# Kernel optimization log

Hardware: AMD Instinct MI355X
Metric: run time of the kernel (lower is better)

## Reference

```python
import math
import jax, jax.numpy as jnp
import numpy as np

HEAD_DIM = 2
ROPE_PERIOD = 19.0
OMEGA = 2.0 * math.pi / ROPE_PERIOD
PEAK_EPS = 0.3
TARGET_LOGIT_GAP = math.log(10.0)
ATTN_AMPLITUDE = TARGET_LOGIT_GAP / (math.cos(OMEGA * PEAK_EPS) - math.cos(OMEGA * (1.0 - PEAK_EPS)))
QK_NORM_SCALE = math.sqrt(ATTN_AMPLITUDE / math.sqrt(2.0))
SCALE = HEAD_DIM ** (-0.5) * QK_NORM_SCALE ** 2
INTERMEDIATE_SIZE = 2
EMBED_CONST = 1000.0
B, L = 4, 4096


def _rms(x, eps=1e-6):
    return x * jax.lax.rsqrt(jnp.mean(x * x, axis=-1, keepdims=True) + eps)


def _rope(x):
    # x: (B, 1, L, 2)
    seq_len = x.shape[2]
    theta = jnp.arange(seq_len, dtype=x.dtype) * jnp.asarray(OMEGA, x.dtype)
    cos_t = jnp.cos(theta)[None, None, :, None]
    sin_t = jnp.sin(theta)[None, None, :, None]
    x0, x1 = x[..., 0:1], x[..., 1:2]
    return jnp.concatenate([x0 * cos_t - x1 * sin_t, x0 * sin_t + x1 * cos_t], axis=-1)


def setup_inputs() -> dict:
    key = jax.random.key(0)
    k1, k2, k3, k4, k5 = jax.random.split(key, 5)
    x = jax.random.normal(k1, (B, L, 2), dtype=jnp.float32)
    # causal additive mask (1, 1, L, L)
    causal = jnp.tril(jnp.ones((L, L), dtype=bool))
    mask = jnp.where(causal, 0.0, -1e9).astype(jnp.float32)[None, None]
    q_weight = jax.random.normal(k2, (1,), dtype=jnp.float32) * 0.1
    v_weight = jax.random.normal(k3, (1,), dtype=jnp.float32) * 0.1
    gate_weight = jax.random.normal(k4, (2,), dtype=jnp.float32) * 0.1
    carry_weight = jax.random.normal(k5, (1,), dtype=jnp.float32) * 0.1
    return {"x": x, "mask": mask, "q_weight": q_weight, "v_weight": v_weight,
            "gate_weight": gate_weight, "carry_weight": carry_weight}


def reference(x, mask, q_weight, v_weight, gate_weight, carry_weight):
    # ---- attention branch ----
    xn = _rms(x)                                    # (B, L, 2)
    phi = q_weight[0]
    q = jnp.stack([xn[..., 0] * jnp.cos(phi), xn[..., 0] * -jnp.sin(phi)], axis=-1)
    k = jnp.stack([xn[..., 0], jnp.zeros_like(xn[..., 0])], axis=-1)
    v = jnp.stack([xn[..., 1] * v_weight[0], jnp.zeros_like(xn[..., 0])], axis=-1)
    q, k, v = q[:, None], k[:, None], v[:, None]    # (B, 1, L, 2)
    q = _rope(_rms(q))
    k = _rope(_rms(k))
    attn = jnp.einsum('bhqd,bhkd->bhqk', q, k) * jnp.asarray(SCALE, x.dtype)
    attn = jax.nn.softmax(attn + mask, axis=-1)
    out = jnp.einsum('bhqk,bhkd->bhqd', attn, v)    # (B, 1, L, 2)
    o0 = out[:, 0, :, 0]                            # (B, L)
    attn_out = jnp.stack([jnp.zeros_like(o0), o0], axis=-1)  # OProj channel swap
    h = x + attn_out
    # ---- gated MLP branch ----
    hn = _rms(h)
    a, c = gate_weight[0], gate_weight[1]
    g0 = hn[..., 0] * a + hn[..., 1] * c
    g1 = hn[..., 0] * (a - c / EMBED_CONST) + hn[..., 1] * c
    base = hn[..., 0]
    mix0 = jax.nn.silu(g0) * base
    mix1 = jax.nn.silu(g1) * base
    y1 = carry_weight[0] * (mix1 - mix0)
    mlp_out = jnp.stack([jnp.zeros_like(y1), y1], axis=-1)
    return h + mlp_out
```

## Files before the change

### kernel.cpp

```cpp
#include <hip/hip_runtime.h>
#include <hip/hip_fp16.h>
#include <math.h>

#define SEQ_L 4096
#define THREADS 512

__device__ __forceinline__ float wave_sum_dpp(float x) {
    int t;
    t = __builtin_amdgcn_update_dpp(0, __float_as_int(x), 0x111, 0xf, 0xf, true); x += __int_as_float(t);
    t = __builtin_amdgcn_update_dpp(0, __float_as_int(x), 0x112, 0xf, 0xf, true); x += __int_as_float(t);
    t = __builtin_amdgcn_update_dpp(0, __float_as_int(x), 0x114, 0xf, 0xf, true); x += __int_as_float(t);
    t = __builtin_amdgcn_update_dpp(0, __float_as_int(x), 0x118, 0xf, 0xf, true); x += __int_as_float(t);
    t = __builtin_amdgcn_update_dpp(0, __float_as_int(x), 0x142, 0xa, 0xf, true); x += __int_as_float(t);
    t = __builtin_amdgcn_update_dpp(0, __float_as_int(x), 0x143, 0xc, 0xf, true); x += __int_as_float(t);
    return x;
}

__device__ __forceinline__ void do_group(
    int g, int lane, const float2* __restrict__ x2, const __half2* aw,
    float2* __restrict__ outp, float scaleL2, float cphi, float sphi,
    float cd, float sd, float ck1, float sk1, float ck2, float sk2,
    float ck3, float sk3, float ga, float gc, float cw)
{
    const float INV19 = 1.0f / 19.0f;
    const float LOG2E = 1.4426950408889634f;

    int m  = g / 19;
    int c  = g - 19 * m;
    int b0 = 76 * m + c;
    int i0r = b0, i1r = b0 + 19, i2r = b0 + 38, i3r = b0 + 57;

    float t2a0, t2a1, t2a2, t2a3, M2a0, M2a1, M2a2, M2a3;
#define ROWINIT(tk, Mk, ik) { \
    int ic_ = (ik) < SEQ_L ? (ik) : (SEQ_L - 1); \
    float2 xv_ = x2[ic_]; \
    float inv_ = __builtin_amdgcn_rsqf(fmaf(xv_.x, xv_.x*0.5f, fmaf(xv_.y, xv_.y*0.5f, 1e-6f))); \
    float xn0_ = xv_.x * inv_; \
    float ai_  = xn0_ * __builtin_amdgcn_rsqf(fmaf(xn0_, xn0_*0.5f, 1e-6f)); \
    tk = scaleL2 * ai_;  Mk = fabsf(tk) * 1.4142135623730951f; }
    ROWINIT(t2a0, M2a0, i0r)
    ROWINIT(t2a1, M2a1, i1r)
    ROWINIT(t2a2, M2a2, i2r)
    ROWINIT(t2a3, M2a3, i3r)
#undef ROWINIT

    unsigned r = (unsigned)(b0 - (lane << 2) + 266) % 19u;
    float rev = (float)r * INV19;
    float crv = __builtin_amdgcn_cosf(rev);
    float srv = __builtin_amdgcn_sinf(rev);
    float C = fmaf(srv, sphi, crv * cphi);
    float S = fmaf(crv, -sphi, srv * cphi);

    float sa0=0.f, sa1=0.f, sa2=0.f, sa3=0.f;
    float oa0=0.f, oa1=0.f, oa2=0.f, oa3=0.f;
    int jb = lane << 2;
    const int ncom = (b0 + 1) >> 8;
    const int i3c  = i3r < SEQ_L ? i3r : (SEQ_L - 1);
    const int T    = (i3c >> 8) + 1;

#define EL(u, pw) { \
    float e0_ = __builtin_amdgcn_exp2f(fmaf(t2a0, (u), -M2a0)); \
    float e1_ = __builtin_amdgcn_exp2f(fmaf(t2a1, (u), -M2a1)); \
    float e2_ = __builtin_amdgcn_exp2f(fmaf(t2a2, (u), -M2a2)); \
    float e3_ = __builtin_amdgcn_exp2f(fmaf(t2a3, (u), -M2a3)); \
    sa0 += e0_; oa0 = fmaf(e0_, (pw), oa0); \
    sa1 += e1_; oa1 = fmaf(e1_, (pw), oa1); \
    sa2 += e2_; oa2 = fmaf(e2_, (pw), oa2); \
    sa3 += e3_; oa3 = fmaf(e3_, (pw), oa3); }
#define ELM(u, pw, jj) { \
    float e0_ = __builtin_amdgcn_exp2f(fmaf(t2a0, (u), -M2a0)); \
    float e1_ = __builtin_amdgcn_exp2f(fmaf(t2a1, (u), -M2a1)); \
    float e2_ = __builtin_amdgcn_exp2f(fmaf(t2a2, (u), -M2a2)); \
    float e3_ = __builtin_amdgcn_exp2f(fmaf(t2a3, (u), -M2a3)); \
    e0_ = ((jj) <= i0r) ? e0_ : 0.f; \
    e1_ = ((jj) <= i1r) ? e1_ : 0.f; \
    e2_ = ((jj) <= i2r) ? e2_ : 0.f; \
    e3_ = ((jj) <= i3r) ? e3_ : 0.f; \
    sa0 += e0_; oa0 = fmaf(e0_, (pw), oa0); \
    sa1 += e1_; oa1 = fmaf(e1_, (pw), oa1); \
    sa2 += e2_; oa2 = fmaf(e2_, (pw), oa2); \
    sa3 += e3_; oa3 = fmaf(e3_, (pw), oa3); }

    int t = 0;
    for (; t < ncom; ++t) {
        float4 raw = *(const float4*)&aw[jb];
        const __half2* hp = (const __half2*)&raw;
        float2 p0 = __half22float2(hp[0]);
        float2 p1 = __half22float2(hp[1]);
        float2 p2 = __half22float2(hp[2]);
        float2 p3 = __half22float2(hp[3]);
        float C1 = fmaf(S, sk1, C * ck1);
        float C2 = fmaf(S, sk2, C * ck2);
        float C3 = fmaf(S, sk3, C * ck3);
        float u0 = p0.x * C,  u1 = p1.x * C1, u2 = p2.x * C2, u3 = p3.x * C3;
        EL(u0, p0.y) EL(u1, p1.y) EL(u2, p2.y) EL(u3, p3.y)
        float Cn = fmaf(S, sd, C * cd);
        float Sn = fmaf(S, cd, -(C * sd));
        C = Cn; S = Sn;
        jb += 256;
    }
    for (; t < T; ++t) {
        float4 raw = *(const float4*)&aw[jb];
        const __half2* hp = (const __half2*)&raw;
        float2 p0 = __half22float2(hp[0]);
        float2 p1 = __half22float2(hp[1]);
        float2 p2 = __half22float2(hp[2]);
        float2 p3 = __half22float2(hp[3]);
        float C1 = fmaf(S, sk1, C * ck1);
        float C2 = fmaf(S, sk2, C * ck2);
        float C3 = fmaf(S, sk3, C * ck3);
        float u0 = p0.x * C,  u1 = p1.x * C1, u2 = p2.x * C2, u3 = p3.x * C3;
        ELM(u0, p0.y, jb)     ELM(u1, p1.y, jb + 1)
        ELM(u2, p2.y, jb + 2) ELM(u3, p3.y, jb + 3)
        float Cn = fmaf(S, sd, C * cd);
        float Sn = fmaf(S, cd, -(C * sd));
        C = Cn; S = Sn;
        jb += 256;
    }
#undef EL
#undef ELM

    float S0 = wave_sum_dpp(sa0), O0 = wave_sum_dpp(oa0);
    float S1 = wave_sum_dpp(sa1), O1 = wave_sum_dpp(oa1);
    float S2 = wave_sum_dpp(sa2), O2 = wave_sum_dpp(oa2);
    float S3 = wave_sum_dpp(sa3), O3 = wave_sum_dpp(oa3);

    if (lane == 63) {
#define EPI(Sk, Ok, ik) if ((ik) < SEQ_L) { \
    float2 xv_ = x2[ik]; \
    float o0_ = (Ok) * __builtin_amdgcn_rcpf(Sk); \
    float h0_ = xv_.x, h1_ = xv_.y + o0_; \
    float inv_ = __builtin_amdgcn_rsqf(fmaf(h0_, h0_*0.5f, fmaf(h1_, h1_*0.5f, 1e-6f))); \
    float hn0_ = h0_ * inv_, hn1_ = h1_ * inv_; \
    float g0_ = hn0_ * ga + hn1_ * gc; \
    float g1_ = hn0_ * (ga - gc * 1e-3f) + hn1_ * gc; \
    float sg0_ = __builtin_amdgcn_rcpf(1.f + __builtin_amdgcn_exp2f(-g0_ * LOG2E)); \
    float sg1_ = __builtin_amdgcn_rcpf(1.f + __builtin_amdgcn_exp2f(-g1_ * LOG2E)); \
    float y1_ = cw * (g1_ * sg1_ - g0_ * sg0_) * hn0_; \
    outp[ik] = make_float2(h0_, h1_ + y1_); }
        EPI(S0, O0, i0r)
        EPI(S1, O1, i1r)
        EPI(S2, O2, i2r)
        EPI(S3, O3, i3r)
#undef EPI
    }
}

__global__ __launch_bounds__(THREADS, 4) void attn_rows_kernel(
    const float* __restrict__ x,
    const float* __restrict__ q_weight,
    const float* __restrict__ v_weight,
    const float* __restrict__ gate_weight,
    const float* __restrict__ carry_weight,
    float* __restrict__ out,
    float scaleL2,
    float cd, float sd,
    float ck1, float sk1, float ck2, float sk2, float ck3, float sk3)
{
    __shared__ __half2 aw[SEQ_L];

    const int tid  = threadIdx.x;
    const int lane = tid & 63;
    const int wave = tid >> 6;
    const int bat  = blockIdx.x >> 7;
    const int bb   = blockIdx.x & 127;

    const float phi = q_weight[0];
    const float vw  = v_weight[0];
    const float2* x2 = (const float2*)x + (size_t)bat * SEQ_L;
    float2* outp = (float2*)out + (size_t)bat * SEQ_L;

    const float INV2PI = 0.15915494309189535f;
    const float rphi = phi * INV2PI;
    const float cphi = __builtin_amdgcn_cosf(rphi);
    const float sphi = __builtin_amdgcn_sinf(rphi);

    for (int j = tid; j < SEQ_L; j += THREADS) {
        float2 xv = x2[j];
        float inv = __builtin_amdgcn_rsqf(
                        fmaf(xv.x, xv.x * 0.5f, fmaf(xv.y, xv.y * 0.5f, 1e-6f)));
        float xn0 = xv.x * inv;
        float xn1 = xv.y * inv;
        float a = xn0 * __builtin_amdgcn_rsqf(fmaf(xn0, xn0 * 0.5f, 1e-6f));
        aw[j] = __floats2half2_rn(a, xn1 * vw);
    }
    __syncthreads();

    const float ga = gate_weight[0];
    const float gc = gate_weight[1];
    const float cw = carry_weight[0];

    const int q = bb + (wave << 7);
    const int g = (q < 513) ? q : (1538 - q);

    do_group(g, lane, x2, aw, outp, scaleL2, cphi, sphi,
             cd, sd, ck1, sk1, ck2, sk2, ck3, sk3, ga, gc, cw);
    if (q == 511)
        do_group(514, lane, x2, aw, outp, scaleL2, cphi, sphi,
                 cd, sd, ck1, sk1, ck2, sk2, ck3, sk3, ga, gc, cw);
    else if (q == 512)
        do_group(513, lane, x2, aw, outp, scaleL2, cphi, sphi,
                 cd, sd, ck1, sk1, ck2, sk2, ck3, sk3, ga, gc, cw);
}

extern "C" void kernel_launch(void* const* d_in, const int* in_sizes, int n_in,
                              void* d_out, int out_size, void* d_ws, size_t ws_size,
                              hipStream_t stream)
{
    const float* x  = (const float*)d_in[0];
    const float* qw = (const float*)d_in[2];
    const float* vw = (const float*)d_in[3];
    const float* gw = (const float*)d_in[4];
    const float* cw = (const float*)d_in[5];
    float* out = (float*)d_out;

    const double omega = 2.0 * M_PI / 19.0;
    const double amp   = log(10.0) / (cos(omega * 0.3) - cos(omega * 0.7));
    const double qkns2 = amp / sqrt(2.0);
    const double scale = pow(2.0, -0.5) * qkns2;
    const double L2E   = 1.4426950408889634074;
    const double delta = 256.0 * omega;

    attn_rows_kernel<<<dim3(4 * 128), dim3(THREADS), 0, stream>>>(
        x, qw, vw, gw, cw, out,
        (float)(scale * L2E),
        (float)cos(delta),       (float)sin(delta),
        (float)cos(omega),       (float)sin(omega),
        (float)cos(2.0 * omega), (float)sin(2.0 * omega),
        (float)cos(3.0 * omega), (float)sin(3.0 * omega));
}
```

Baseline: 18.41 us.

## Store keys and values as fp32 in LDS, pair rows per wave, prefetch tiles

Changes the per-key LDS table from packed half2 to two padded fp32 arrays, removing half-to-float conversions and fp16 rounding. Each wave now handles two complementary row groups (b0 and 4046-b0) so causal work is balanced, and blocks shrink to 256 threads with 129 blocks per batch. The loop software-prefetches the next float4 tile, and row init reads the precomputed normalized values from LDS. In exchange, LDS use doubles and the input staging is done in fewer, wider loads.

```diff
diff --git a/kernel.cpp b/kernel.cpp
--- a/kernel.cpp
+++ b/kernel.cpp
@@ -1,9 +1,8 @@
 #include <hip/hip_runtime.h>
-#include <hip/hip_fp16.h>
 #include <math.h>
 
 #define SEQ_L 4096
-#define THREADS 512
+#define LDS_PAD 260
 
 __device__ __forceinline__ float wave_sum_dpp(float x) {
     int t;
@@ -17,35 +16,28 @@
 }
 
 __device__ __forceinline__ void do_group(
-    int g, int lane, const float2* __restrict__ x2, const __half2* aw,
-    float2* __restrict__ outp, float scaleL2, float cphi, float sphi,
+    int b0, int lane, const float2* __restrict__ x2,
+    const float* As, const float* Ws, float2* __restrict__ outp,
+    float scaleL2, float cphi, float sphi,
     float cd, float sd, float ck1, float sk1, float ck2, float sk2,
     float ck3, float sk3, float ga, float gc, float cw)
 {
-    const float INV19 = 1.0f / 19.0f;
     const float LOG2E = 1.4426950408889634f;
-
-    int m  = g / 19;
-    int c  = g - 19 * m;
-    int b0 = 76 * m + c;
-    int i0r = b0, i1r = b0 + 19, i2r = b0 + 38, i3r = b0 + 57;
-
-    float t2a0, t2a1, t2a2, t2a3, M2a0, M2a1, M2a2, M2a3;
-#define ROWINIT(tk, Mk, ik) { \
-    int ic_ = (ik) < SEQ_L ? (ik) : (SEQ_L - 1); \
-    float2 xv_ = x2[ic_]; \
-    float inv_ = __builtin_amdgcn_rsqf(fmaf(xv_.x, xv_.x*0.5f, fmaf(xv_.y, xv_.y*0.5f, 1e-6f))); \
-    float xn0_ = xv_.x * inv_; \
-    float ai_  = xn0_ * __builtin_amdgcn_rsqf(fmaf(xn0_, xn0_*0.5f, 1e-6f)); \
-    tk = scaleL2 * ai_;  Mk = fabsf(tk) * 1.4142135623730951f; }
-    ROWINIT(t2a0, M2a0, i0r)
-    ROWINIT(t2a1, M2a1, i1r)
-    ROWINIT(t2a2, M2a2, i2r)
-    ROWINIT(t2a3, M2a3, i3r)
-#undef ROWINIT
+    const float SQRT2 = 1.4142135623730951f;
+    const int i0 = b0, i1 = b0 + 19, i2 = b0 + 38, i3 = b0 + 57;
+    const int c1 = i1 < SEQ_L ? i1 : SEQ_L - 1;
+    const int c2 = i2 < SEQ_L ? i2 : SEQ_L - 1;
+    const int c3 = i3 < SEQ_L ? i3 : SEQ_L - 1;
+
+    const float t20 = scaleL2 * As[i0], t21 = scaleL2 * As[c1];
+    const float t22 = scaleL2 * As[c2], t23 = scaleL2 * As[c3];
+    const float M20 = fabsf(t20) * SQRT2, M21 = fabsf(t21) * SQRT2;
+    const float M22 = fabsf(t22) * SQRT2, M23 = fabsf(t23) * SQRT2;
+
+    const float2 xv0 = x2[i0], xv1 = x2[c1], xv2 = x2[c2], xv3 = x2[c3];
 
     unsigned r = (unsigned)(b0 - (lane << 2) + 266) % 19u;
-    float rev = (float)r * INV19;
+    float rev = (float)r * (1.0f / 19.0f);
     float crv = __builtin_amdgcn_cosf(rev);
     float srv = __builtin_amdgcn_sinf(rev);
     float C = fmaf(srv, sphi, crv * cphi);
@@ -55,70 +47,66 @@
     float oa0=0.f, oa1=0.f, oa2=0.f, oa3=0.f;
     int jb = lane << 2;
     const int ncom = (b0 + 1) >> 8;
-    const int i3c  = i3r < SEQ_L ? i3r : (SEQ_L - 1);
-    const int T    = (i3c >> 8) + 1;
-
-#define EL(u, pw) { \
-    float e0_ = __builtin_amdgcn_exp2f(fmaf(t2a0, (u), -M2a0)); \
-    float e1_ = __builtin_amdgcn_exp2f(fmaf(t2a1, (u), -M2a1)); \
-    float e2_ = __builtin_amdgcn_exp2f(fmaf(t2a2, (u), -M2a2)); \
-    float e3_ = __builtin_amdgcn_exp2f(fmaf(t2a3, (u), -M2a3)); \
+    const int T    = (c3 >> 8) + 1;
+
+#define EL4(u, pw) { \
+    float e0_ = __builtin_amdgcn_exp2f(fmaf(t20, (u), -M20)); \
+    float e1_ = __builtin_amdgcn_exp2f(fmaf(t21, (u), -M21)); \
+    float e2_ = __builtin_amdgcn_exp2f(fmaf(t22, (u), -M22)); \
+    float e3_ = __builtin_amdgcn_exp2f(fmaf(t23, (u), -M23)); \
     sa0 += e0_; oa0 = fmaf(e0_, (pw), oa0); \
     sa1 += e1_; oa1 = fmaf(e1_, (pw), oa1); \
     sa2 += e2_; oa2 = fmaf(e2_, (pw), oa2); \
     sa3 += e3_; oa3 = fmaf(e3_, (pw), oa3); }
-#define ELM(u, pw, jj) { \
-    float e0_ = __builtin_amdgcn_exp2f(fmaf(t2a0, (u), -M2a0)); \
-    float e1_ = __builtin_amdgcn_exp2f(fmaf(t2a1, (u), -M2a1)); \
-    float e2_ = __builtin_amdgcn_exp2f(fmaf(t2a2, (u), -M2a2)); \
-    float e3_ = __builtin_amdgcn_exp2f(fmaf(t2a3, (u), -M2a3)); \
-    e0_ = ((jj) <= i0r) ? e0_ : 0.f; \
-    e1_ = ((jj) <= i1r) ? e1_ : 0.f; \
-    e2_ = ((jj) <= i2r) ? e2_ : 0.f; \
-    e3_ = ((jj) <= i3r) ? e3_ : 0.f; \
+#define ELM4(u, pw, jj) { \
+    float e0_ = __builtin_amdgcn_exp2f(fmaf(t20, (u), -M20)); \
+    float e1_ = __builtin_amdgcn_exp2f(fmaf(t21, (u), -M21)); \
+    float e2_ = __builtin_amdgcn_exp2f(fmaf(t22, (u), -M22)); \
+    float e3_ = __builtin_amdgcn_exp2f(fmaf(t23, (u), -M23)); \
+    e0_ = ((jj) <= i0) ? e0_ : 0.f; \
+    e1_ = ((jj) <= i1) ? e1_ : 0.f; \
+    e2_ = ((jj) <= i2) ? e2_ : 0.f; \
+    e3_ = ((jj) <= i3) ? e3_ : 0.f; \
     sa0 += e0_; oa0 = fmaf(e0_, (pw), oa0); \
     sa1 += e1_; oa1 = fmaf(e1_, (pw), oa1); \
     sa2 += e2_; oa2 = fmaf(e2_, (pw), oa2); \
     sa3 += e3_; oa3 = fmaf(e3_, (pw), oa3); }
-
+#define ROT() { \
+    float Cn_ = fmaf(S, sd, C * cd); \
+    float Sn_ = fmaf(S, cd, -(C * sd)); \
+    C = Cn_; S = Sn_; }
+
+    float4 av = *(const float4*)&As[jb];
+    float4 wv = *(const float4*)&Ws[jb];
     int t = 0;
     for (; t < ncom; ++t) {
-        float4 raw = *(const float4*)&aw[jb];
-        const __half2* hp = (const __half2*)&raw;
-        float2 p0 = __half22float2(hp[0]);
-        float2 p1 = __half22float2(hp[1]);
-        float2 p2 = __half22float2(hp[2]);
-        float2 p3 = __half22float2(hp[3]);
+        float4 avn = *(const float4*)&As[jb + 256];
+        float4 wvn = *(const float4*)&Ws[jb + 256];
         float C1 = fmaf(S, sk1, C * ck1);
         float C2 = fmaf(S, sk2, C * ck2);
         float C3 = fmaf(S, sk3, C * ck3);
-        float u0 = p0.x * C,  u1 = p1.x * C1, u2 = p2.x * C2, u3 = p3.x * C3;
-        EL(u0, p0.y) EL(u1, p1.y) EL(u2, p2.y) EL(u3, p3.y)
-        float Cn = fmaf(S, sd, C * cd);
-        float Sn = fmaf(S, cd, -(C * sd));
-        C = Cn; S = Sn;
-        jb += 256;
+        float u0 = av.x * C,  u1 = av.y * C1;
+        float u2 = av.z * C2, u3 = av.w * C3;
+        EL4(u0, wv.x) EL4(u1, wv.y) EL4(u2, wv.z) EL4(u3, wv.w)
+        ROT();
+        av = avn; wv = wvn; jb += 256;
     }
     for (; t < T; ++t) {
-        float4 raw = *(const float4*)&aw[jb];
-        const __half2* hp = (const __half2*)&raw;
-        float2 p0 = __half22float2(hp[0]);
-        float2 p1 = __half22float2(hp[1]);
-        float2 p2 = __half22float2(hp[2]);
-        float2 p3 = __half22float2(hp[3]);
+        float4 avn = *(const float4*)&As[jb + 256];
+        float4 wvn = *(const float4*)&Ws[jb + 256];
         float C1 = fmaf(S, sk1, C * ck1);
         float C2 = fmaf(S, sk2, C * ck2);
         float C3 = fmaf(S, sk3, C * ck3);
-        float u0 = p0.x * C,  u1 = p1.x * C1, u2 = p2.x * C2, u3 = p3.x * C3;
-        ELM(u0, p0.y, jb)     ELM(u1, p1.y, jb + 1)
-        ELM(u2, p2.y, jb + 2) ELM(u3, p3.y, jb + 3)
-        float Cn = fmaf(S, sd, C * cd);
-        float Sn = fmaf(S, cd, -(C * sd));
-        C = Cn; S = Sn;
-        jb += 256;
-    }
-#undef EL
-#undef ELM
+        float u0 = av.x * C,  u1 = av.y * C1;
+        float u2 = av.z * C2, u3 = av.w * C3;
+        ELM4(u0, wv.x, jb)     ELM4(u1, wv.y, jb + 1)
+        ELM4(u2, wv.z, jb + 2) ELM4(u3, wv.w, jb + 3)
+        ROT();
+        av = avn; wv = wvn; jb += 256;
+    }
+#undef EL4
+#undef ELM4
+#undef ROT
 
     float S0 = wave_sum_dpp(sa0), O0 = wave_sum_dpp(oa0);
     float S1 = wave_sum_dpp(sa1), O1 = wave_sum_dpp(oa1);
@@ -126,10 +114,9 @@
     float S3 = wave_sum_dpp(sa3), O3 = wave_sum_dpp(oa3);
 
     if (lane == 63) {
-#define EPI(Sk, Ok, ik) if ((ik) < SEQ_L) { \
-    float2 xv_ = x2[ik]; \
+#define EPI(Sk, Ok, ik, xvk) if ((ik) < SEQ_L) { \
     float o0_ = (Ok) * __builtin_amdgcn_rcpf(Sk); \
-    float h0_ = xv_.x, h1_ = xv_.y + o0_; \
+    float h0_ = (xvk).x, h1_ = (xvk).y + o0_; \
     float inv_ = __builtin_amdgcn_rsqf(fmaf(h0_, h0_*0.5f, fmaf(h1_, h1_*0.5f, 1e-6f))); \
     float hn0_ = h0_ * inv_, hn1_ = h1_ * inv_; \
     float g0_ = hn0_ * ga + hn1_ * gc; \
@@ -138,15 +125,15 @@
     float sg1_ = __builtin_amdgcn_rcpf(1.f + __builtin_amdgcn_exp2f(-g1_ * LOG2E)); \
     float y1_ = cw * (g1_ * sg1_ - g0_ * sg0_) * hn0_; \
     outp[ik] = make_float2(h0_, h1_ + y1_); }
-        EPI(S0, O0, i0r)
-        EPI(S1, O1, i1r)
-        EPI(S2, O2, i2r)
-        EPI(S3, O3, i3r)
+        EPI(S0, O0, i0, xv0)
+        EPI(S1, O1, i1, xv1)
+        EPI(S2, O2, i2, xv2)
+        EPI(S3, O3, i3, xv3)
 #undef EPI
     }
 }
 
-__global__ __launch_bounds__(THREADS, 4) void attn_rows_kernel(
+__global__ __launch_bounds__(256, 4) void attn_rows_kernel(
     const float* __restrict__ x,
     const float* __restrict__ q_weight,
     const float* __restrict__ v_weight,
@@ -157,13 +144,14 @@
     float cd, float sd,
     float ck1, float sk1, float ck2, float sk2, float ck3, float sk3)
 {
-    __shared__ __half2 aw[SEQ_L];
+    __shared__ float As[SEQ_L + LDS_PAD];
+    __shared__ float Ws[SEQ_L + LDS_PAD];
 
     const int tid  = threadIdx.x;
     const int lane = tid & 63;
     const int wave = tid >> 6;
-    const int bat  = blockIdx.x >> 7;
-    const int bb   = blockIdx.x & 127;
+    const int bat  = blockIdx.x / 129;
+    const int bb   = blockIdx.x % 129;
 
     const float phi = q_weight[0];
     const float vw  = v_weight[0];
@@ -175,32 +163,39 @@
     const float cphi = __builtin_amdgcn_cosf(rphi);
     const float sphi = __builtin_amdgcn_sinf(rphi);
 
-    for (int j = tid; j < SEQ_L; j += THREADS) {
-        float2 xv = x2[j];
-        float inv = __builtin_amdgcn_rsqf(
-                        fmaf(xv.x, xv.x * 0.5f, fmaf(xv.y, xv.y * 0.5f, 1e-6f)));
-        float xn0 = xv.x * inv;
-        float xn1 = xv.y * inv;
-        float a = xn0 * __builtin_amdgcn_rsqf(fmaf(xn0, xn0 * 0.5f, 1e-6f));
-        aw[j] = __floats2half2_rn(a, xn1 * vw);
+    const float4* x4 = (const float4*)x2;
+    #pragma unroll
+    for (int it = 0; it < 8; ++it) {
+        int idx = tid + (it << 8);
+        float4 v = x4[idx];
+        int e0 = idx << 1, e1 = e0 + 1;
+        float inv0 = __builtin_amdgcn_rsqf(fmaf(v.x, v.x*0.5f, fmaf(v.y, v.y*0.5f, 1e-6f)));
+        float xn0a = v.x * inv0;
+        As[e0] = xn0a * __builtin_amdgcn_rsqf(fmaf(xn0a, xn0a*0.5f, 1e-6f));
+        Ws[e0] = v.y * inv0 * vw;
+        float inv1 = __builtin_amdgcn_rsqf(fmaf(v.z, v.z*0.5f, fmaf(v.w, v.w*0.5f, 1e-6f)));
+        float xn0b = v.z * inv1;
+        As[e1] = xn0b * __builtin_amdgcn_rsqf(fmaf(xn0b, xn0b*0.5f, 1e-6f));
+        Ws[e1] = v.w * inv1 * vw;
     }
     __syncthreads();
+
+    const int p = bb * 4 + wave;
+    if (p >= 513) return;
 
     const float ga = gate_weight[0];
     const float gc = gate_weight[1];
     const float cw = carry_weight[0];
 
-    const int q = bb + (wave << 7);
-    const int g = (q < 513) ? q : (1538 - q);
-
-    do_group(g, lane, x2, aw, outp, scaleL2, cphi, sphi,
+    const int m = p / 19;
+    const int c = p - 19 * m;
+    const int b0A = 76 * m + c;
+    const int b0B = 4046 - b0A;
+
+    do_group(b0A, lane, x2, As, Ws, outp, scaleL2, cphi, sphi,
              cd, sd, ck1, sk1, ck2, sk2, ck3, sk3, ga, gc, cw);
-    if (q == 511)
-        do_group(514, lane, x2, aw, outp, scaleL2, cphi, sphi,
-                 cd, sd, ck1, sk1, ck2, sk2, ck3, sk3, ga, gc, cw);
-    else if (q == 512)
-        do_group(513, lane, x2, aw, outp, scaleL2, cphi, sphi,
-                 cd, sd, ck1, sk1, ck2, sk2, ck3, sk3, ga, gc, cw);
+    do_group(b0B, lane, x2, As, Ws, outp, scaleL2, cphi, sphi,
+             cd, sd, ck1, sk1, ck2, sk2, ck3, sk3, ga, gc, cw);
 }
 
 extern "C" void kernel_launch(void* const* d_in, const int* in_sizes, int n_in,
@@ -221,7 +216,7 @@
     const double L2E   = 1.4426950408889634074;
     const double delta = 256.0 * omega;
 
-    attn_rows_kernel<<<dim3(4 * 128), dim3(THREADS), 0, stream>>>(
+    attn_rows_kernel<<<dim3(4 * 129), dim3(256), 0, stream>>>(
         x, qw, vw, gw, cw, out,
         (float)(scale * L2E),
         (float)cos(delta),       (float)sin(delta),
```

Measured after the change: 18.32 us. Within noise of the previous version (-0.5%).
